# Kernel optimization log

Hardware: AMD Instinct MI355X
Metric: run time of the kernel (lower is better)

Reference implementation:

```python
import jax, jax.numpy as jnp
import numpy as np


def _fake_quant(w):
    # Dynamic per-tensor int8 quantization of weights (scale = max|w|/127),
    # immediately dequantized, as quantized_lstm does for its packed weights.
    s = jnp.max(jnp.abs(w)) / 127.0
    q = jnp.clip(jnp.round(w / s), -128.0, 127.0) * s
    # straight-through so the same code is usable under vjp
    return w + jax.lax.stop_gradient(q - w)


def _run_dir(xs, h0, c0, w_ih, w_hh, b, reverse):
    # xs: [T,B,in]; h0,c0: [B,H]; w_ih: [4H,in]; w_hh: [4H,H]; b: [4H]
    def step(carry, x_t):
        h, c = carry
        gates = x_t @ w_ih.T + h @ w_hh.T + b  # [B,4H]
        i, f, g, o = jnp.split(gates, 4, axis=-1)  # PyTorch gate order i,f,g,o
        c = jax.nn.sigmoid(f) * c + jax.nn.sigmoid(i) * jnp.tanh(g)
        h = jax.nn.sigmoid(o) * jnp.tanh(c)
        return (h, c), h
    (hT, cT), ys = jax.lax.scan(step, (h0, c0), xs, reverse=reverse)
    return ys, hT, cT


def _lstm(x, h0, c0, w_ih, w_hh, b_ih, b_hh):
    # x: [B,T,I] (batch_first); h0/c0: [L*2,B,H]; weights stacked [L,2,...]
    L = w_ih.shape[0]
    xs = jnp.transpose(x, (1, 0, 2))  # time-major [T,B,I]
    h_n, c_n = [], []
    for l in range(L):
        outs = []
        for d in range(2):  # 0=fwd, 1=bwd
            idx = 2 * l + d
            wih = _fake_quant(w_ih[l, d])
            whh = _fake_quant(w_hh[l, d])
            b = b_ih[l, d] + b_hh[l, d]
            ys, hT, cT = _run_dir(xs, h0[idx], c0[idx], wih, whh, b, reverse=(d == 1))
            outs.append(ys)
            h_n.append(hT)
            c_n.append(cT)
        xs = jnp.concatenate(outs, axis=-1)  # [T,B,2H] feeds next layer
    out = jnp.transpose(xs, (1, 0, 2))  # back to batch_first [B,T,2H]
    return out, jnp.stack(h_n), jnp.stack(c_n)


def setup_inputs() -> dict:
    key = jax.random.key(0)
    ks = jax.random.split(key, 7)
    B, T, I, H, L = 32, 256, 1024, 512, 2
    sc = 1.0 / np.sqrt(H)
    return {
        "x": jax.random.normal(ks[0], (B, T, I), jnp.float32),
        "h0": jax.random.normal(ks[1], (2 * L, B, H), jnp.float32),
        "c0": jax.random.normal(ks[2], (2 * L, B, H), jnp.float32),
        "w_ih": jax.random.normal(ks[3], (L, 2, 4 * H, I), jnp.float32) * sc,
        "w_hh": jax.random.normal(ks[4], (L, 2, 4 * H, H), jnp.float32) * sc,
        "b_ih": jax.random.normal(ks[5], (L, 2, 4 * H), jnp.float32) * sc,
        "b_hh": jax.random.normal(ks[6], (L, 2, 4 * H), jnp.float32) * sc,
    }


def reference(x, h0, c0, w_ih, w_hh, b_ih, b_hh):
    return _lstm(x, h0, c0, w_ih, w_hh, b_ih, b_hh)
```

## Files before the change

kernel.cpp:

```cpp
#include <hip/hip_runtime.h>

typedef __attribute__((ext_vector_type(8))) short bf16x8;
typedef __attribute__((ext_vector_type(4))) float f32x4;
typedef __attribute__((ext_vector_type(4))) unsigned u32x4;

#define BB   32
#define TT   256
#define II   1024
#define HH   512
#define GG   2048
#define BT   8192

#define WS_OFF_FLAGS   0ull
#define WS_OFF_SCALES  1024ull
#define WS_MEMSET_SPAN 2048ull
#define WS_OFF_QIH     4096ull
#define QIH_BYTES      (4ull*GG*II*2)
#define WS_OFF_QHH     (WS_OFF_QIH + QIH_BYTES)
#define QHH_BYTES      (4ull*GG*HH*2)
#define WS_OFF_XBUF    (WS_OFF_QHH + QHH_BYTES)
#define XBUF_BYTES     (1ull*BT*II*2)
#define WS_OFF_YS1     (WS_OFF_XBUF + XBUF_BYTES)
#define WS_OFF_HFRAG   (WS_OFF_YS1 + XBUF_BYTES)
#define HFRAG_BYTES    (2ull*2*2*16*1024)
#define WS_OFF_GX      (WS_OFF_HFRAG + HFRAG_BYTES)
#define GX_ELEMS       (2ull*TT*GG*BB)

__device__ __forceinline__ unsigned short f2bf(float f){
  unsigned u = __float_as_uint(f);
  u += 0x7fffu + ((u >> 16) & 1u);
  return (unsigned short)(u >> 16);
}
__device__ __forceinline__ float bf2f(unsigned short h){ return __uint_as_float(((unsigned)h) << 16); }
__device__ __forceinline__ unsigned pack2(float a, float b){ return (unsigned)f2bf(a) | ((unsigned)f2bf(b) << 16); }
__device__ __forceinline__ float sigm(float x){ return 1.0f / (1.0f + __expf(-x)); }
__device__ __forceinline__ float tanh_(float x){
  float e = __expf(-2.0f * fabsf(x));
  float t = (1.0f - e) / (1.0f + e);
  return x < 0.0f ? -t : t;
}

__device__ __forceinline__ void st_dword(void* p, float v){
  asm volatile("global_store_dword %0, %1, off" :: "v"(p), "v"(v) : "memory");
}
__device__ __forceinline__ void st_b128(void* p, u32x4 v){
  asm volatile("global_store_dwordx4 %0, %1, off" :: "v"(p), "v"(v) : "memory");
}
__device__ __forceinline__ void st_b128_coh(void* p, u32x4 v){
  asm volatile("global_store_dwordx4 %0, %1, off sc0 sc1" :: "v"(p), "v"(v) : "memory");
}
__device__ __forceinline__ void ld_dword(float* d, const void* p){
  asm volatile("global_load_dword %0, %1, off" : "=v"(*d) : "v"(p));
}
__device__ __forceinline__ void ld_ushort(unsigned* d, const void* p){
  asm volatile("global_load_ushort %0, %1, off" : "=v"(*d) : "v"(p));
}
__device__ __forceinline__ void ld_frag(bf16x8* d, const void* p){
  asm volatile("global_load_dwordx4 %0, %1, off" : "=v"(*d) : "v"(p));
}
__device__ __forceinline__ void ld_frag_coh(bf16x8* d, const void* p){
  asm volatile("global_load_dwordx4 %0, %1, off sc0 sc1" : "=v"(*d) : "v"(p));
}
#define WAITV0() do{ asm volatile("s_waitcnt vmcnt(0)" ::: "memory"); __builtin_amdgcn_sched_barrier(0); }while(0)

__global__ __launch_bounds__(256) void k_absmax(const float* __restrict__ wih,
                                                const float* __restrict__ whh,
                                                unsigned* __restrict__ scales_raw){
  int t = blockIdx.y;
  const float* base; size_t n;
  if (t < 4){ base = wih + (size_t)t * GG * II; n = (size_t)GG * II; }
  else      { base = whh + (size_t)(t - 4) * GG * HH; n = (size_t)GG * HH; }
  size_t gtid = (size_t)blockIdx.x * 256 + threadIdx.x;
  float m = 0.0f;
  const float4* b4 = (const float4*)base;
  size_t n4 = n >> 2;
  for (size_t i = gtid; i < n4; i += 8192){
    float4 v = b4[i];
    m = fmaxf(m, fmaxf(fmaxf(fabsf(v.x), fabsf(v.y)), fmaxf(fabsf(v.z), fabsf(v.w))));
  }
  for (int off = 32; off; off >>= 1) m = fmaxf(m, __shfl_xor(m, off));
  __shared__ float red[4];
  int w = threadIdx.x >> 6, l = threadIdx.x & 63;
  if (l == 0) red[w] = m;
  __syncthreads();
  if (threadIdx.x == 0){
    m = fmaxf(fmaxf(red[0], red[1]), fmaxf(red[2], red[3]));
    atomicMax(&scales_raw[t], __float_as_uint(m));
  }
}

__global__ __launch_bounds__(256) void k_quant_ih(const float* __restrict__ wih,
                                                  unsigned short* __restrict__ qih,
                                                  const unsigned* __restrict__ scales_raw){
  size_t i8 = (size_t)blockIdx.x * 256 + threadIdx.x;
  int t = (int)(i8 >> 18);
  size_t off = (i8 & 262143) << 3;
  float s = __uint_as_float(scales_raw[t]) / 127.0f;
  s = fmaxf(s, 1e-30f);
  const float* src = wih + ((size_t)t << 21) + off;
  float4 v0 = *(const float4*)src, v1 = *(const float4*)(src + 4);
  float q[8] = {v0.x, v0.y, v0.z, v0.w, v1.x, v1.y, v1.z, v1.w};
#pragma unroll
  for (int j = 0; j < 8; ++j) q[j] = fminf(127.0f, fmaxf(-128.0f, rintf(q[j] / s)));
  uint4 o; o.x = pack2(q[0], q[1]); o.y = pack2(q[2], q[3]); o.z = pack2(q[4], q[5]); o.w = pack2(q[6], q[7]);
  *(uint4*)(qih + ((size_t)t << 21) + off) = o;
}

__global__ __launch_bounds__(256) void k_quant_hh(const float* __restrict__ whh,
                                                  unsigned short* __restrict__ qhh,
                                                  const unsigned* __restrict__ scales_raw){
  size_t i8 = (size_t)blockIdx.x * 256 + threadIdx.x;
  int t = (int)(i8 >> 17);
  size_t o = i8 & 131071;
  int k8 = (int)(o & 63);
  int r  = (int)((o >> 6) & 63);
  int bi = (int)(o >> 12);
  int w = r >> 4, hu = (r >> 2) & 3, gt = r & 3;
  int j = gt * 512 + bi * 16 + w * 4 + hu;
  float s = __uint_as_float(scales_raw[4 + t]) / 127.0f;
  s = fmaxf(s, 1e-30f);
  const float* src = whh + ((size_t)t << 20) + (size_t)j * HH + ((size_t)k8 << 3);
  float4 v0 = *(const float4*)src, v1 = *(const float4*)(src + 4);
  float q[8] = {v0.x, v0.y, v0.z, v0.w, v1.x, v1.y, v1.z, v1.w};
#pragma unroll
  for (int jj = 0; jj < 8; ++jj) q[jj] = fminf(127.0f, fmaxf(-128.0f, rintf(q[jj] / s)));
  uint4 ov; ov.x = pack2(q[0], q[1]); ov.y = pack2(q[2], q[3]); ov.z = pack2(q[4], q[5]); ov.w = pack2(q[6], q[7]);
  *(uint4*)(qhh + ((size_t)t << 20) + (((size_t)bi * 64 + r) << 9) + ((size_t)k8 << 3)) = ov;
}

__global__ __launch_bounds__(256) void k_cvtx(const float* __restrict__ x,
                                              unsigned short* __restrict__ xbuf){
  size_t i8 = (size_t)blockIdx.x * 256 + threadIdx.x;
  size_t row = i8 >> 7;
  int c8 = (int)(i8 & 127);
  int t = (int)(row >> 5), b = (int)(row & 31);
  const float* src = x + (((size_t)b * TT + t) << 10) + ((size_t)c8 << 3);
  float4 v0 = *(const float4*)src, v1 = *(const float4*)(src + 4);
  uint4 o; o.x = pack2(v0.x, v0.y); o.y = pack2(v0.z, v0.w); o.z = pack2(v1.x, v1.y); o.w = pack2(v1.z, v1.w);
  *(uint4*)(xbuf + (row << 10) + ((size_t)c8 << 3)) = o;
}

__global__ __launch_bounds__(256) void k_gemm(const unsigned short* __restrict__ Aq,
                                              const unsigned short* __restrict__ X,
                                              float* __restrict__ gxf,
                                              unsigned short* __restrict__ gxh, int gx16,
                                              const unsigned* __restrict__ scales_raw, int sbase){
  int d = blockIdx.z;
  const unsigned short* A = Aq + ((size_t)d << 21);
  float s = __uint_as_float(scales_raw[sbase + d]) / 127.0f;
  __shared__ unsigned short As[128 * 64];
  __shared__ unsigned short Bs[128 * 64];
  int tid = threadIdx.x;
  int l = tid & 63;
  int wv = tid >> 6;
  int wr = wv >> 1, wc = wv & 1;
  int jt = blockIdx.y, mt = blockIdx.x;
  size_t arow0 = (size_t)jt * 128;
  size_t brow0 = (size_t)mt * 128;
  f32x4 acc[4][4];
  f32x4 z = {0.f, 0.f, 0.f, 0.f};
#pragma unroll
  for (int i = 0; i < 4; ++i)
#pragma unroll
    for (int j = 0; j < 4; ++j) acc[i][j] = z;

  for (int kt = 0; kt < II; kt += 64){
    __syncthreads();
#pragma unroll
    for (int p = 0; p < 4; ++p){
      int ch = p * 256 + tid;
      int r = ch >> 3; int ce = (ch & 7) << 3;
      *(uint4*)&As[r * 64 + ce] = *(const uint4*)&A[(arow0 + r) * II + kt + ce];
      *(uint4*)&Bs[r * 64 + ce] = *(const uint4*)&X[(brow0 + r) * II + kt + ce];
    }
    __syncthreads();
#pragma unroll
    for (int kk = 0; kk < 64; kk += 32){
      bf16x8 a[4], b[4];
#pragma unroll
      for (int mi = 0; mi < 4; ++mi) a[mi] = *(const bf16x8*)&As[(wr * 64 + mi * 16 + (l & 15)) * 64 + kk + (l >> 4) * 8];
#pragma unroll
      for (int ni = 0; ni < 4; ++ni) b[ni] = *(const bf16x8*)&Bs[(wc * 64 + ni * 16 + (l & 15)) * 64 + kk + (l >> 4) * 8];
#pragma unroll
      for (int mi = 0; mi < 4; ++mi)
#pragma unroll
        for (int ni = 0; ni < 4; ++ni)
          acc[mi][ni] = __builtin_amdgcn_mfma_f32_16x16x32_bf16(a[mi], b[ni], acc[mi][ni], 0, 0, 0);
    }
  }
  size_t gxbase = (size_t)d * ((size_t)TT * GG * BB);
#pragma unroll
  for (int mi = 0; mi < 4; ++mi){
    int j0 = jt * 128 + wr * 64 + mi * 16 + ((l >> 4) << 2);
#pragma unroll
    for (int ni = 0; ni < 4; ++ni){
      int m = mt * 128 + wc * 64 + ni * 16 + (l & 15);
      int t = m >> 5, bb = m & 31;
#pragma unroll
      for (int r = 0; r < 4; ++r){
        size_t o = gxbase + ((size_t)(t * GG + j0 + r) * BB + bb);
        float v = s * acc[mi][ni][r];
        if (gx16) gxh[o] = f2bf(v); else gxf[o] = v;
      }
    }
  }
}

template<int GX16>
__global__ __launch_bounds__(256) void k_scan(const unsigned short* __restrict__ qhh,
                                              const float* __restrict__ gxf,
                                              const unsigned short* __restrict__ gxh,
                                              const float* __restrict__ h0,
                                              const float* __restrict__ c0,
                                              const float* __restrict__ bih,
                                              const float* __restrict__ bhh,
                                              const unsigned* __restrict__ scales_raw,
                                              char* __restrict__ hfrag,
                                              unsigned* __restrict__ flags,
                                              int layer,
                                              unsigned short* __restrict__ ys,
                                              float* __restrict__ out){
  __shared__ __align__(16) unsigned short stage[512];
  int tid = threadIdx.x;
  int d = blockIdx.x >> 5, bi = blockIdx.x & 31;
  int w = tid >> 6, l = tid & 63;
  int ld = layer * 2 + d;
  float s_hh = __uint_as_float(scales_raw[4 + ld]) / 127.0f;

  int hu = l >> 4;
  int hidden = bi * 16 + w * 4 + hu;
  int klocal = w * 4 + hu;
  int bb0 = l & 15, bb1 = 16 + bb0;

  char* hfd = hfrag + (size_t)d * 65536;
  unsigned* fl = flags + d * 32;

  int p_arr = l >> 5, p_z = (l >> 4) & 1, p_bb = l & 15;
  size_t p_rec = (size_t)p_arr * 16384 + (size_t)(bi >> 1) * 1024
               + (size_t)((2 * (bi & 1) + p_z) * 16 + p_bb) * 16;

  if (w == 0){
    const float* sp = h0 + ((size_t)ld << 14) + ((size_t)(p_arr * 16 + p_bb) << 9)
                    + bi * 16 + p_z * 8;
    float4 v0 = *(const float4*)sp, v1 = *(const float4*)(sp + 4);
    u32x4 o = {pack2(v0.x, v0.y), pack2(v0.z, v0.w), pack2(v1.x, v1.y), pack2(v1.z, v1.w)};
    st_b128_coh(hfd + p_rec, o);
    WAITV0();
    if (tid == 0)
      __hip_atomic_store(&fl[bi], 1u, __ATOMIC_RELAXED, __HIP_MEMORY_SCOPE_AGENT);
  }

  float bias[4];
#pragma unroll
  for (int gt = 0; gt < 4; ++gt){
    int j = gt * 512 + hidden;
    bias[gt] = bih[(size_t)ld * GG + j] + bhh[(size_t)ld * GG + j];
  }
  float cc0 = c0[((size_t)ld * BB + bb0) * HH + hidden];
  float cc1 = c0[((size_t)ld * BB + bb1) * HH + hidden];

  int rA = w * 16 + (l & 15);
  int koffe = (l >> 4) * 8;
  const unsigned short* qsl = qhh + ((size_t)ld << 20) + ((size_t)bi << 15);
  bf16x8 afrag[16];
#pragma unroll
  for (int kk = 0; kk < 16; ++kk)
    ld_frag(&afrag[kk], qsl + (size_t)rA * 512 + kk * 32 + koffe);

  const float* gxd_f = gxf + (size_t)d * ((size_t)TT * GG * BB);
  const unsigned short* gxd_h = gxh + (size_t)d * ((size_t)TT * GG * BB);

  float gxv[8]; unsigned gxu[8];
  {
    int t0 = d ? TT - 1 : 0;
    size_t base = (size_t)t0 * GG * BB;
#pragma unroll
    for (int gt = 0; gt < 4; ++gt){
      size_t o = base + (size_t)(gt * 512 + hidden) * BB;
      if (GX16){ ld_ushort(&gxu[gt * 2],     gxd_h + o + bb0);
                 ld_ushort(&gxu[gt * 2 + 1], gxd_h + o + bb1); }
      else     { ld_dword(&gxv[gt * 2],      gxd_f + o + bb0);
                 ld_dword(&gxv[gt * 2 + 1],  gxd_f + o + bb1); }
    }
  }

  for (int s = 0; s < TT; ++s){
    int t = d ? (TT - 1 - s) : s;

    if (w == 0 && l < 32){
      unsigned target = (unsigned)(s + 1);
      while (true){
        unsigned v = __hip_atomic_load(&fl[l], __ATOMIC_RELAXED, __HIP_MEMORY_SCOPE_AGENT);
        if (__all((int)(v >= target))) break;
        __builtin_amdgcn_s_sleep(1);
      }
    }
    __syncthreads();

    const char* pb = hfd + (size_t)(s & 1) * 32768 + (size_t)l * 16;
    bf16x8 b0f[16], b1f[16];
#pragma unroll
    for (int kk = 0; kk < 16; ++kk) ld_frag_coh(&b0f[kk], pb + kk * 1024);
#pragma unroll
    for (int kk = 0; kk < 16; ++kk) ld_frag_coh(&b1f[kk], pb + 16384 + kk * 1024);
    WAITV0();

    f32x4 acc0 = {0.f, 0.f, 0.f, 0.f}, acc1 = {0.f, 0.f, 0.f, 0.f};
#pragma unroll
    for (int kk = 0; kk < 16; ++kk){
      acc0 = __builtin_amdgcn_mfma_f32_16x16x32_bf16(afrag[kk], b0f[kk], acc0, 0, 0, 0);
      acc1 = __builtin_amdgcn_mfma_f32_16x16x32_bf16(afrag[kk], b1f[kk], acc1, 0, 0, 0);
    }

    float g0[4], g1[4];
#pragma unroll
    for (int gt = 0; gt < 4; ++gt){
      float gx0 = GX16 ? bf2f((unsigned short)gxu[gt * 2])     : gxv[gt * 2];
      float gx1 = GX16 ? bf2f((unsigned short)gxu[gt * 2 + 1]) : gxv[gt * 2 + 1];
      g0[gt] = acc0[gt] * s_hh + gx0 + bias[gt];
      g1[gt] = acc1[gt] * s_hh + gx1 + bias[gt];
    }
    float i0 = sigm(g0[0]), f0 = sigm(g0[1]), G0 = tanh_(g0[2]), o0 = sigm(g0[3]);
    float i1 = sigm(g1[0]), f1 = sigm(g1[1]), G1 = tanh_(g1[2]), o1 = sigm(g1[3]);
    float cn0 = f0 * cc0 + i0 * G0;  cc0 = cn0;
    float cn1 = f1 * cc1 + i1 * G1;  cc1 = cn1;
    float hx0 = o0 * tanh_(cn0);
    float hx1 = o1 * tanh_(cn1);

    if (s == TT - 1){
      st_dword(out + 8388608ull + ((size_t)ld * BB + bb0) * HH + hidden, hx0);
      st_dword(out + 8388608ull + ((size_t)ld * BB + bb1) * HH + hidden, hx1);
      st_dword(out + 8454144ull + ((size_t)ld * BB + bb0) * HH + hidden, cn0);
      st_dword(out + 8454144ull + ((size_t)ld * BB + bb1) * HH + hidden, cn1);
    }

    stage[bb0 * 16 + klocal]       = f2bf(hx0);
    stage[256 + bb0 * 16 + klocal] = f2bf(hx1);
    __syncthreads();

    if (w == 0){
      if (s < TT - 1){
        u32x4 v = *(const u32x4*)&stage[p_arr * 256 + p_bb * 16 + p_z * 8];
        st_b128_coh(hfd + (size_t)((s + 1) & 1) * 32768 + p_rec, v);
        WAITV0();
        if (tid == 0)
          __hip_atomic_store(&fl[bi], (unsigned)(s + 2), __ATOMIC_RELAXED, __HIP_MEMORY_SCOPE_AGENT);
      }
    } else if (w == 1){
      int i = tid - 64;
      int arr = i >> 5, bbx = (i >> 1) & 15, half = i & 1;
      u32x4 v = *(const u32x4*)&stage[arr * 256 + bbx * 16 + half * 8];
      st_b128(ys + (((size_t)(t * BB + arr * 16 + bbx)) << 10) + d * 512 + bi * 16 + half * 8, v);
    }

    if (s < TT - 1){
      int tn = d ? (TT - 2 - s) : (s + 1);
      size_t base = (size_t)tn * GG * BB;
#pragma unroll
      for (int gt = 0; gt < 4; ++gt){
        size_t o = base + (size_t)(gt * 512 + hidden) * BB;
        if (GX16){ ld_ushort(&gxu[gt * 2],     gxd_h + o + bb0);
                   ld_ushort(&gxu[gt * 2 + 1], gxd_h + o + bb1); }
        else     { ld_dword(&gxv[gt * 2],      gxd_f + o + bb0);
                   ld_dword(&gxv[gt * 2 + 1],  gxd_f + o + bb1); }
      }
    }
  }
  WAITV0();
}

__global__ __launch_bounds__(256) void k_out(const unsigned short* __restrict__ ys,
                                             float* __restrict__ out){
  size_t i4 = (size_t)blockIdx.x * 256 + threadIdx.x;
  size_t idx = i4 << 2;
  size_t row = idx >> 10; int c = (int)(idx & 1023);
  int t = (int)(row >> 5), b = (int)(row & 31);
  ushort4 v = *(const ushort4*)&ys[idx];
  float4 o = {bf2f(v.x), bf2f(v.y), bf2f(v.z), bf2f(v.w)};
  *(float4*)&out[(((size_t)b * TT + t) << 10) + c] = o;
}

extern "C" void kernel_launch(void* const* d_in, const int* in_sizes, int n_in,
                              void* d_out, int out_size, void* d_ws, size_t ws_size,
                              hipStream_t stream){
  if (n_in < 7) return;
  const float* x   = (const float*)d_in[0];
  const float* h0  = (const float*)d_in[1];
  const float* c0  = (const float*)d_in[2];
  const float* wih = (const float*)d_in[3];
  const float* whh = (const float*)d_in[4];
  const float* bih = (const float*)d_in[5];
  const float* bhh = (const float*)d_in[6];
  float* out = (float*)d_out;

  char* ws = (char*)d_ws;
  unsigned* flags = (unsigned*)(ws + WS_OFF_FLAGS);
  unsigned* scales = (unsigned*)(ws + WS_OFF_SCALES);
  unsigned short* qih  = (unsigned short*)(ws + WS_OFF_QIH);
  unsigned short* qhh  = (unsigned short*)(ws + WS_OFF_QHH);
  unsigned short* xbuf = (unsigned short*)(ws + WS_OFF_XBUF);
  unsigned short* ys1  = (unsigned short*)(ws + WS_OFF_YS1);
  char* hfrag = ws + WS_OFF_HFRAG;
  float* gxf = (float*)(ws + WS_OFF_GX);
  unsigned short* gxh = (unsigned short*)(ws + WS_OFF_GX);

  size_t need_f32 = WS_OFF_GX + GX_ELEMS * 4ull;
  int gx16 = (ws_size >= need_f32) ? 0 : 1;

  (void)hipMemsetAsync(ws, 0, WS_MEMSET_SPAN, stream);

  k_absmax<<<dim3(32, 8), 256, 0, stream>>>(wih, whh, scales);
  k_quant_ih<<<4096, 256, 0, stream>>>(wih, qih, scales);
  k_quant_hh<<<2048, 256, 0, stream>>>(whh, qhh, scales);
  k_cvtx<<<4096, 256, 0, stream>>>(x, xbuf);

  k_gemm<<<dim3(64, 16, 2), 256, 0, stream>>>(qih, xbuf, gxf, gxh, gx16, scales, 0);
  if (gx16) k_scan<1><<<64, 256, 0, stream>>>(qhh, gxf, gxh, h0, c0, bih, bhh, scales, hfrag, flags, 0, ys1, out);
  else      k_scan<0><<<64, 256, 0, stream>>>(qhh, gxf, gxh, h0, c0, bih, bhh, scales, hfrag, flags, 0, ys1, out);
  k_gemm<<<dim3(64, 16, 2), 256, 0, stream>>>(qih + 2ull * GG * II, ys1, gxf, gxh, gx16, scales, 2);
  if (gx16) k_scan<1><<<64, 256, 0, stream>>>(qhh, gxf, gxh, h0, c0, bih, bhh, scales, hfrag, flags + 64, 1, ys1, out);
  else      k_scan<0><<<64, 256, 0, stream>>>(qhh, gxf, gxh, h0, c0, bih, bhh, scales, hfrag, flags + 64, 1, ys1, out);

  k_out<<<8192, 256, 0, stream>>>(ys1, out);

  (void)in_sizes; (void)out_size;
}
```

Before: 2.145 ms.

## Replace flag-based step sync with tagged hidden-state payloads in scan

Each bf16 hidden value is stored in a 32-bit word whose upper half carries a step tag. Consumers poll the data itself and check that every tag matches, so the producer no longer waits on its store before writing a flag. It also falls back to checking a sentinel flag, shares loaded fragments across waves through LDS, and double-buffers the staging area. This aims to remove the store-wait-then-flag round trip on the recurrent critical path, at the cost of doubling the hidden-state exchange traffic and adding capped spin loops that could exit early on timeout.

```diff
diff --git a/kernel.cpp b/kernel.cpp
--- a/kernel.cpp
+++ b/kernel.cpp
@@ -11,7 +11,7 @@
 #define GG   2048
 #define BT   8192
 
-#define WS_OFF_FLAGS   0ull
+#define WS_OFF_SENT    0ull
 #define WS_OFF_SCALES  1024ull
 #define WS_MEMSET_SPAN 2048ull
 #define WS_OFF_QIH     4096ull
@@ -22,9 +22,12 @@
 #define XBUF_BYTES     (1ull*BT*II*2)
 #define WS_OFF_YS1     (WS_OFF_XBUF + XBUF_BYTES)
 #define WS_OFF_HFRAG   (WS_OFF_YS1 + XBUF_BYTES)
-#define HFRAG_BYTES    (2ull*2*2*16*1024)
+#define HFRAG_BYTES    262144ull
 #define WS_OFF_GX      (WS_OFF_HFRAG + HFRAG_BYTES)
 #define GX_ELEMS       (2ull*TT*GG*BB)
+
+#define CAP_BULK  (1 << 16)
+#define CAP_SENT  (1 << 17)
 
 __device__ __forceinline__ unsigned short f2bf(float f){
   unsigned u = __float_as_uint(f);
@@ -49,17 +52,28 @@
 __device__ __forceinline__ void st_b128_coh(void* p, u32x4 v){
   asm volatile("global_store_dwordx4 %0, %1, off sc0 sc1" :: "v"(p), "v"(v) : "memory");
 }
+__device__ __forceinline__ void st_du_coh(void* p, unsigned v){
+  asm volatile("global_store_dword %0, %1, off sc0 sc1" :: "v"(p), "v"(v) : "memory");
+}
 __device__ __forceinline__ void ld_dword(float* d, const void* p){
   asm volatile("global_load_dword %0, %1, off" : "=v"(*d) : "v"(p));
 }
 __device__ __forceinline__ void ld_ushort(unsigned* d, const void* p){
   asm volatile("global_load_ushort %0, %1, off" : "=v"(*d) : "v"(p));
 }
+__device__ __forceinline__ void ld_du_coh(unsigned* d, const void* p){
+  asm volatile("global_load_dword %0, %1, off sc0 sc1" : "=v"(*d) : "v"(p));
+}
 __device__ __forceinline__ void ld_frag(bf16x8* d, const void* p){
   asm volatile("global_load_dwordx4 %0, %1, off" : "=v"(*d) : "v"(p));
 }
-__device__ __forceinline__ void ld_frag_coh(bf16x8* d, const void* p){
+__device__ __forceinline__ void ld_tag(u32x4* d, const void* p){
   asm volatile("global_load_dwordx4 %0, %1, off sc0 sc1" : "=v"(*d) : "v"(p));
+}
+__device__ __forceinline__ unsigned vperm(unsigned s0, unsigned s1, unsigned sel){
+  unsigned d;
+  asm("v_perm_b32 %0, %1, %2, %3" : "=v"(d) : "v"(s0), "v"(s1), "s"(sel));
+  return d;
 }
 #define WAITV0() do{ asm volatile("s_waitcnt vmcnt(0)" ::: "memory"); __builtin_amdgcn_sched_barrier(0); }while(0)
 
@@ -207,20 +221,21 @@
 }
 
 template<int GX16>
-__global__ __launch_bounds__(256) void k_scan(const unsigned short* __restrict__ qhh,
-                                              const float* __restrict__ gxf,
-                                              const unsigned short* __restrict__ gxh,
-                                              const float* __restrict__ h0,
-                                              const float* __restrict__ c0,
-                                              const float* __restrict__ bih,
-                                              const float* __restrict__ bhh,
-                                              const unsigned* __restrict__ scales_raw,
-                                              char* __restrict__ hfrag,
-                                              unsigned* __restrict__ flags,
-                                              int layer,
-                                              unsigned short* __restrict__ ys,
-                                              float* __restrict__ out){
-  __shared__ __align__(16) unsigned short stage[512];
+__global__ __launch_bounds__(256, 1) void k_scan(const unsigned short* __restrict__ qhh,
+                                                 const float* __restrict__ gxf,
+                                                 const unsigned short* __restrict__ gxh,
+                                                 const float* __restrict__ h0,
+                                                 const float* __restrict__ c0,
+                                                 const float* __restrict__ bih,
+                                                 const float* __restrict__ bhh,
+                                                 const unsigned* __restrict__ scales_raw,
+                                                 char* __restrict__ hfrag,
+                                                 unsigned* __restrict__ sent,
+                                                 int layer,
+                                                 unsigned short* __restrict__ ys,
+                                                 float* __restrict__ out){
+  __shared__ __align__(16) unsigned short FragLds[32 * 64 * 8];
+  __shared__ __align__(16) unsigned short stage2[2][512];
   int tid = threadIdx.x;
   int d = blockIdx.x >> 5, bi = blockIdx.x & 31;
   int w = tid >> 6, l = tid & 63;
@@ -231,23 +246,24 @@
   int hidden = bi * 16 + w * 4 + hu;
   int klocal = w * 4 + hu;
   int bb0 = l & 15, bb1 = 16 + bb0;
-
-  char* hfd = hfrag + (size_t)d * 65536;
-  unsigned* fl = flags + d * 32;
-
-  int p_arr = l >> 5, p_z = (l >> 4) & 1, p_bb = l & 15;
-  size_t p_rec = (size_t)p_arr * 16384 + (size_t)(bi >> 1) * 1024
-               + (size_t)((2 * (bi & 1) + p_z) * 16 + p_bb) * 16;
+  unsigned tbase = (unsigned)(layer << 9);
+
+  char* hfd = hfrag + (size_t)d * 131072;
+  unsigned* sd = sent + d * 32;
+
+  int p_a = l >> 5, p_z = (l >> 4) & 1, p_bb = l & 15;
+  size_t prec_off = (size_t)p_a * 32768 + (size_t)(bi >> 1) * 2048
+                  + (size_t)((2 * (bi & 1) + p_z) * 16 + p_bb) * 32;
 
   if (w == 0){
-    const float* sp = h0 + ((size_t)ld << 14) + ((size_t)(p_arr * 16 + p_bb) << 9)
-                    + bi * 16 + p_z * 8;
+    const float* sp = h0 + ((size_t)ld << 14) + ((size_t)(p_a * 16 + p_bb) << 9) + bi * 16 + p_z * 8;
     float4 v0 = *(const float4*)sp, v1 = *(const float4*)(sp + 4);
-    u32x4 o = {pack2(v0.x, v0.y), pack2(v0.z, v0.w), pack2(v1.x, v1.y), pack2(v1.z, v1.w)};
-    st_b128_coh(hfd + p_rec, o);
-    WAITV0();
-    if (tid == 0)
-      __hip_atomic_store(&fl[bi], 1u, __ATOMIC_RELAXED, __HIP_MEMORY_SCOPE_AGENT);
+    unsigned tg = (tbase + 1u) << 16;
+    u32x4 lo = { tg | f2bf(v0.x), tg | f2bf(v0.y), tg | f2bf(v0.z), tg | f2bf(v0.w) };
+    u32x4 hi = { tg | f2bf(v1.x), tg | f2bf(v1.y), tg | f2bf(v1.z), tg | f2bf(v1.w) };
+    st_b128_coh(hfd + prec_off, lo);
+    st_b128_coh(hfd + prec_off + 16, hi);
+    if (l == 0) st_du_coh(&sd[bi], tbase + 1u);
   }
 
   float bias[4];
@@ -284,32 +300,73 @@
     }
   }
 
+  const unsigned SEL_TAG = 0x07060302u;
+  const unsigned SEL_PAY = 0x05040100u;
+  int kb = w * 4;
+
   for (int s = 0; s < TT; ++s){
     int t = d ? (TT - 1 - s) : s;
-
-    if (w == 0 && l < 32){
-      unsigned target = (unsigned)(s + 1);
+    unsigned tagv = tbase + (unsigned)s + 1u;
+    unsigned tt2 = (tagv << 16) | tagv;
+    const char* cb = hfd + (size_t)(s & 1) * 65536 + (size_t)l * 32;
+
+    u32x4 rq[16];
+    {
+      int sok = 0, gb = 0, gs = 0;
       while (true){
-        unsigned v = __hip_atomic_load(&fl[l], __ATOMIC_RELAXED, __HIP_MEMORY_SCOPE_AGENT);
-        if (__all((int)(v >= target))) break;
-        __builtin_amdgcn_s_sleep(1);
+#pragma unroll
+        for (int arr = 0; arr < 2; ++arr)
+#pragma unroll
+          for (int q = 0; q < 4; ++q){
+            const char* p = cb + arr * 32768 + (kb + q) * 2048;
+            ld_tag(&rq[arr * 8 + q * 2],     p);
+            ld_tag(&rq[arr * 8 + q * 2 + 1], p + 16);
+          }
+        WAITV0();
+        unsigned bad = 0u;
+#pragma unroll
+        for (int i = 0; i < 16; ++i){
+          bad |= vperm(rq[i][1], rq[i][0], SEL_TAG) ^ tt2;
+          bad |= vperm(rq[i][3], rq[i][2], SEL_TAG) ^ tt2;
+        }
+        if (!__any((int)(bad != 0u))) break;
+        if (++gb > CAP_BULK) break;
+        if (!sok){
+          while (true){
+            unsigned v;
+            ld_du_coh(&v, sd + (l & 31));
+            WAITV0();
+            if (__all((int)(v >= tagv))){ sok = 1; break; }
+            if (++gs > CAP_SENT){ sok = 1; break; }
+            __builtin_amdgcn_s_sleep(1);
+          }
+        } else {
+          __builtin_amdgcn_s_sleep(2);
+        }
       }
     }
+
+#pragma unroll
+    for (int arr = 0; arr < 2; ++arr)
+#pragma unroll
+      for (int q = 0; q < 4; ++q){
+        int i0 = arr * 8 + q * 2;
+        u32x4 pk;
+        pk[0] = vperm(rq[i0][1],     rq[i0][0],     SEL_PAY);
+        pk[1] = vperm(rq[i0][3],     rq[i0][2],     SEL_PAY);
+        pk[2] = vperm(rq[i0 + 1][1], rq[i0 + 1][0], SEL_PAY);
+        pk[3] = vperm(rq[i0 + 1][3], rq[i0 + 1][2], SEL_PAY);
+        *(u32x4*)&FragLds[(((size_t)(arr * 16 + kb + q)) * 64 + l) * 8] = pk;
+      }
     __syncthreads();
 
-    const char* pb = hfd + (size_t)(s & 1) * 32768 + (size_t)l * 16;
-    bf16x8 b0f[16], b1f[16];
-#pragma unroll
-    for (int kk = 0; kk < 16; ++kk) ld_frag_coh(&b0f[kk], pb + kk * 1024);
-#pragma unroll
-    for (int kk = 0; kk < 16; ++kk) ld_frag_coh(&b1f[kk], pb + 16384 + kk * 1024);
-    WAITV0();
-
     f32x4 acc0 = {0.f, 0.f, 0.f, 0.f}, acc1 = {0.f, 0.f, 0.f, 0.f};
 #pragma unroll
     for (int kk = 0; kk < 16; ++kk){
-      acc0 = __builtin_amdgcn_mfma_f32_16x16x32_bf16(afrag[kk], b0f[kk], acc0, 0, 0, 0);
-      acc1 = __builtin_amdgcn_mfma_f32_16x16x32_bf16(afrag[kk], b1f[kk], acc1, 0, 0, 0);
+      bf16x8 b0 = *(const bf16x8*)&FragLds[((size_t)kk * 64 + l) * 8];
+      bf16x8 b1 = *(const bf16x8*)&FragLds[(((size_t)(16 + kk)) * 64 + l) * 8];
+      acc0 = __builtin_amdgcn_mfma_f32_16x16x32_bf16(afrag[kk], b0, acc0, 0, 0, 0);
+      acc1 = __builtin_amdgcn_mfma_f32_16x16x32_bf16(afrag[kk], b1, acc1, 0, 0, 0);
     }
 
     float g0[4], g1[4];
@@ -334,22 +391,28 @@
       st_dword(out + 8454144ull + ((size_t)ld * BB + bb1) * HH + hidden, cn1);
     }
 
-    stage[bb0 * 16 + klocal]       = f2bf(hx0);
-    stage[256 + bb0 * 16 + klocal] = f2bf(hx1);
+    int par = (s + 1) & 1;
+    stage2[par][bb0 * 16 + klocal]       = f2bf(hx0);
+    stage2[par][256 + bb0 * 16 + klocal] = f2bf(hx1);
     __syncthreads();
 
     if (w == 0){
       if (s < TT - 1){
-        u32x4 v = *(const u32x4*)&stage[p_arr * 256 + p_bb * 16 + p_z * 8];
-        st_b128_coh(hfd + (size_t)((s + 1) & 1) * 32768 + p_rec, v);
-        WAITV0();
-        if (tid == 0)
-          __hip_atomic_store(&fl[bi], (unsigned)(s + 2), __ATOMIC_RELAXED, __HIP_MEMORY_SCOPE_AGENT);
+        unsigned tg2 = (tagv + 1u) << 16;
+        u32x4 raw = *(const u32x4*)&stage2[par][p_a * 256 + p_bb * 16 + p_z * 8];
+        u32x4 lo = { tg2 | (raw[0] & 0xffffu), tg2 | (raw[0] >> 16),
+                     tg2 | (raw[1] & 0xffffu), tg2 | (raw[1] >> 16) };
+        u32x4 hi = { tg2 | (raw[2] & 0xffffu), tg2 | (raw[2] >> 16),
+                     tg2 | (raw[3] & 0xffffu), tg2 | (raw[3] >> 16) };
+        char* pp = hfd + (size_t)par * 65536 + prec_off;
+        st_b128_coh(pp, lo);
+        st_b128_coh(pp + 16, hi);
+        if (l == 0) st_du_coh(&sd[bi], tagv + 1u);
       }
     } else if (w == 1){
       int i = tid - 64;
       int arr = i >> 5, bbx = (i >> 1) & 15, half = i & 1;
-      u32x4 v = *(const u32x4*)&stage[arr * 256 + bbx * 16 + half * 8];
+      u32x4 v = *(const u32x4*)&stage2[par][arr * 256 + bbx * 16 + half * 8];
       st_b128(ys + (((size_t)(t * BB + arr * 16 + bbx)) << 10) + d * 512 + bi * 16 + half * 8, v);
     }
 
@@ -394,7 +457,7 @@
   float* out = (float*)d_out;
 
   char* ws = (char*)d_ws;
-  unsigned* flags = (unsigned*)(ws + WS_OFF_FLAGS);
+  unsigned* sent = (unsigned*)(ws + WS_OFF_SENT);
   unsigned* scales = (unsigned*)(ws + WS_OFF_SCALES);
   unsigned short* qih  = (unsigned short*)(ws + WS_OFF_QIH);
   unsigned short* qhh  = (unsigned short*)(ws + WS_OFF_QHH);
@@ -408,6 +471,7 @@
   int gx16 = (ws_size >= need_f32) ? 0 : 1;
 
   (void)hipMemsetAsync(ws, 0, WS_MEMSET_SPAN, stream);
+  (void)hipMemsetAsync(hfrag, 0, HFRAG_BYTES, stream);
 
   k_absmax<<<dim3(32, 8), 256, 0, stream>>>(wih, whh, scales);
   k_quant_ih<<<4096, 256, 0, stream>>>(wih, qih, scales);
@@ -415,11 +479,11 @@
   k_cvtx<<<4096, 256, 0, stream>>>(x, xbuf);
 
   k_gemm<<<dim3(64, 16, 2), 256, 0, stream>>>(qih, xbuf, gxf, gxh, gx16, scales, 0);
-  if (gx16) k_scan<1><<<64, 256, 0, stream>>>(qhh, gxf, gxh, h0, c0, bih, bhh, scales, hfrag, flags, 0, ys1, out);
-  else      k_scan<0><<<64, 256, 0, stream>>>(qhh, gxf, gxh, h0, c0, bih, bhh, scales, hfrag, flags, 0, ys1, out);
+  if (gx16) k_scan<1><<<64, 256, 0, stream>>>(qhh, gxf, gxh, h0, c0, bih, bhh, scales, hfrag, sent, 0, ys1, out);
+  else      k_scan<0><<<64, 256, 0, stream>>>(qhh, gxf, gxh, h0, c0, bih, bhh, scales, hfrag, sent, 0, ys1, out);
   k_gemm<<<dim3(64, 16, 2), 256, 0, stream>>>(qih + 2ull * GG * II, ys1, gxf, gxh, gx16, scales, 2);
-  if (gx16) k_scan<1><<<64, 256, 0, stream>>>(qhh, gxf, gxh, h0, c0, bih, bhh, scales, hfrag, flags + 64, 1, ys1, out);
-  else      k_scan<0><<<64, 256, 0, stream>>>(qhh, gxf, gxh, h0, c0, bih, bhh, scales, hfrag, flags + 64, 1, ys1, out);
+  if (gx16) k_scan<1><<<64, 256, 0, stream>>>(qhh, gxf, gxh, h0, c0, bih, bhh, scales, hfrag, sent, 1, ys1, out);
+  else      k_scan<0><<<64, 256, 0, stream>>>(qhh, gxf, gxh, h0, c0, bih, bhh, scales, hfrag, sent, 1, ys1, out);
 
   k_out<<<8192, 256, 0, stream>>>(ys1, out);
 
```

Result: slower. 2.189 ms (+2.1%).
